# Kernel optimization log

Measured on AMD Instinct MI355X. Metric: run time of the kernel, lower is better.

The kernel has to match this reference:

```python
import jax, jax.numpy as jnp
import numpy as np
import math

LMAX = 2
NUM_Z = 4
N_NODES = 20000
N_GRAPHS = 5000
N_EDGES = 320000
# irreps as (mul, l, parity)
IR_SH   = [(1, 0, 1), (1, 1, -1), (1, 2, 1)]
IR_ATTR = [(NUM_Z**2, 0, 1), (NUM_Z**2, 1, -1), (NUM_Z**2, 2, 1)]
IR_MID  = [(64, 0, 1), (24, 1, 1), (24, 1, -1), (16, 2, 1), (16, 2, -1)]
IR_OUT  = [(1, 0, -1), (6, 0, 1)]


def _cg(j1, j2, j3, m1, m2, m3):
    if m1 + m2 != m3:
        return 0.0
    f = math.factorial
    pre = math.sqrt((2 * j3 + 1) * f(j3 + j1 - j2) * f(j3 - j1 + j2) * f(j1 + j2 - j3) / f(j1 + j2 + j3 + 1))
    pre *= math.sqrt(f(j3 + m3) * f(j3 - m3) * f(j1 - m1) * f(j1 + m1) * f(j2 - m2) * f(j2 + m2))
    s = 0.0
    for k in range(max(0, j2 - j3 - m1, j1 - j3 + m2), min(j1 + j2 - j3, j1 - m1, j2 + m2) + 1):
        s += (-1) ** k / (f(k) * f(j1 + j2 - j3 - k) * f(j1 - m1 - k) * f(j2 + m2 - k) * f(j3 - j2 + m1 + k) * f(j3 - j1 - m2 + k))
    return pre * s


def _u(l):
    # complex -> real spherical harmonics change of basis, m = -l..l
    U = np.zeros((2 * l + 1, 2 * l + 1), dtype=complex)
    for m in range(-l, l + 1):
        if m > 0:
            U[m + l, -m + l] = 1 / math.sqrt(2)
            U[m + l, m + l] = (-1) ** m / math.sqrt(2)
        elif m == 0:
            U[l, l] = 1.0
        else:
            U[m + l, m + l] = 1j / math.sqrt(2)
            U[m + l, -m + l] = -1j * (-1) ** (-m) / math.sqrt(2)
    return U


def _w3j(l1, l2, l3):
    C = np.zeros((2 * l1 + 1, 2 * l2 + 1, 2 * l3 + 1))
    for m1 in range(-l1, l1 + 1):
        for m2 in range(-l2, l2 + 1):
            m3 = m1 + m2
            if -l3 <= m3 <= l3:
                C[m1 + l1, m2 + l2, m3 + l3] = _cg(l1, l2, l3, m1, m2, m3)
    T = np.einsum('am,bn,co,mno->abc', _u(l1), _u(l2), _u(l3).conj(), C.astype(complex))
    T = T.real if np.abs(T.real).max() >= np.abs(T.imag).max() else T.imag
    return (T / np.linalg.norm(T)).astype(np.float32)  # Frobenius norm 1, e3nn convention


W3J = {(a, b, c): _w3j(a, b, c) for a in range(3) for b in range(3) for c in range(3) if abs(a - b) <= c <= a + b}


def _slices(ir):
    s = [0]
    for m, l, _ in ir:
        s.append(s[-1] + m * (2 * l + 1))
    return s


def _paths(ir1, ir2, iro):
    paths = []
    fan = [0] * len(iro)
    off = 0
    for a, (m1, l1, p1) in enumerate(ir1):
        for b, (m2, l2, p2) in enumerate(ir2):
            for c, (m3, l3, p3) in enumerate(iro):
                if p1 * p2 == p3 and abs(l1 - l2) <= l3 <= l1 + l2:
                    paths.append((a, b, c, off))
                    fan[c] += m1 * m2
                    off += m1 * m2 * m3
    return paths, fan, off


def _fctp(x1, x2, w, ir1, ir2, iro):
    # FullyConnectedTensorProduct: 'uvw' weighted Clebsch-Gordan contraction per path
    s1, s2 = _slices(ir1), _slices(ir2)
    paths, fan, _ = _paths(ir1, ir2, iro)
    E = x1.shape[0]
    out = [jnp.zeros((E, m * (2 * l + 1)), x1.dtype) for m, l, _ in iro]
    for a, b, c, off in paths:
        m1, l1, _ = ir1[a]
        m2, l2, _ = ir2[b]
        m3, l3, _ = iro[c]
        W = w[off:off + m1 * m2 * m3].reshape(m1, m2, m3)
        C = jnp.asarray(W3J[(l1, l2, l3)], x1.dtype)
        xa = x1[:, s1[a]:s1[a + 1]].reshape(E, m1, 2 * l1 + 1)
        xb = x2[:, s2[b]:s2[b + 1]].reshape(E, m2, 2 * l2 + 1)
        alpha = math.sqrt(2 * l3 + 1) / math.sqrt(fan[c])
        y = jnp.einsum('eui,evj,ijk,uvw->ewk', xa, xb, C, W)
        out[c] = out[c] + (alpha * y).reshape(E, -1)
    return jnp.concatenate(out, axis=1)


def _sh(v):
    # component-normalized harmonic polynomials for l=0,1,2 (normalize=False)
    x, y, z = v[:, 0], v[:, 1], v[:, 2]
    r2 = x * x + y * y + z * z
    s3, s15, s5 = math.sqrt(3.0), math.sqrt(15.0), math.sqrt(5.0)
    sh1 = s3 * jnp.stack([y, z, x], axis=1)
    sh2 = jnp.stack([s15 * x * y, s15 * y * z, 0.5 * s5 * (3 * z * z - r2), s15 * x * z, 0.5 * s15 * (x * x - y * y)], axis=1)
    return jnp.concatenate([jnp.ones_like(x)[:, None], sh1, sh2], axis=1)  # [E, 9]


def _forward(pos, w_tp1, w_tp2, z, batch, edge_src, edge_dst):
    E = edge_src.shape[0]
    ev = pos[edge_src] - pos[edge_dst]
    sh = _sh(ev)
    zz = NUM_Z * z[edge_src] + z[edge_dst]
    zzf = jax.nn.one_hot(zz, NUM_Z ** 2, dtype=sh.dtype) * NUM_Z  # [E, 16]
    # 'uvu' TensorProduct of (16x0e) with sh: outer product per l block
    blocks = [(0, 1), (1, 4), (4, 9)]
    edge_attr = jnp.concatenate([(zzf[:, :, None] * sh[:, None, a:b]).reshape(E, -1) for a, b in blocks], axis=1)
    inv_nn = 1.0 / math.sqrt(3.0)  # num_neighbors = 3
    node = jax.ops.segment_sum(sh, edge_dst, num_segments=N_NODES) * inv_nn
    ef = _fctp(node[edge_src], edge_attr, w_tp1, IR_SH, IR_ATTR, IR_MID)
    node = jax.ops.segment_sum(ef, edge_dst, num_segments=N_NODES) * inv_nn
    ef = _fctp(node[edge_src], edge_attr, w_tp2, IR_MID, IR_ATTR, IR_OUT)
    node = jax.ops.segment_sum(ef, edge_dst, num_segments=N_NODES) * inv_nn
    return jax.ops.segment_sum(node, batch, num_segments=N_GRAPHS) * 0.5  # num_nodes = 4


def setup_inputs() -> dict:
    key = jax.random.key(0)
    k = jax.random.split(key, 7)
    _, _, n1 = _paths(IR_SH, IR_ATTR, IR_MID)
    _, _, n2 = _paths(IR_MID, IR_ATTR, IR_OUT)
    return {
        'pos': jax.random.normal(k[0], (N_NODES, 3), jnp.float32),
        'z': jax.random.randint(k[1], (N_NODES,), 0, NUM_Z, jnp.int32),
        'batch': jnp.sort(jax.random.randint(k[2], (N_NODES,), 0, N_GRAPHS, jnp.int32)),
        'edge_src': jax.random.randint(k[3], (N_EDGES,), 0, N_NODES, jnp.int32),
        'edge_dst': jax.random.randint(k[4], (N_EDGES,), 0, N_NODES, jnp.int32),
        'w_tp1': jax.random.normal(k[5], (n1,), jnp.float32),
        'w_tp2': jax.random.normal(k[6], (n2,), jnp.float32),
    }


def reference(pos, z, batch, edge_src, edge_dst, w_tp1, w_tp2):
    return _forward(pos, w_tp1, w_tp2, z, batch, edge_src, edge_dst)
```

## Files before the change

### kernel.cpp

```cpp
#include <hip/hip_runtime.h>


#define N_EDGES   320000
#define NN_NODES  20000
#define NN_GRAPHS 5000

__device__ __forceinline__ void sh_from_vec(float x, float y, float z,
                                            float* B1, float* B2) {
    const float s3   = 1.7320508075688772f;
    const float s15  = 3.8729833462074170f;
    const float s5h  = 1.1180339887498949f;
    const float s15h = 1.9364916731037085f;
    B1[0] = s3 * y; B1[1] = s3 * z; B1[2] = s3 * x;
    float r2 = x * x + y * y + z * z;
    B2[0] = s15 * x * y;
    B2[1] = s15 * y * z;
    B2[2] = s5h * (3.f * z * z - r2);
    B2[3] = s15 * x * z;
    B2[4] = s15h * (x * x - y * y);
}

__global__ __launch_bounds__(256) void k_zero(const float* __restrict__ pos,
                                              int* __restrict__ counts,
                                              float* __restrict__ out,
                                              float4* __restrict__ pos4) {
    int tid = blockIdx.x * blockDim.x + threadIdx.x;
    int stride = gridDim.x * blockDim.x;
    for (int i = tid; i < NN_NODES; i += stride) counts[i] = 0;
    for (int i = tid; i < NN_GRAPHS * 7; i += stride) out[i] = 0.f;
    for (int i = tid; i < NN_NODES; i += stride) {
        float4 p;
        p.x = pos[3 * i]; p.y = pos[3 * i + 1]; p.z = pos[3 * i + 2]; p.w = 0.f;
        pos4[i] = p;
    }
}

__global__ __launch_bounds__(256) void k_hist(const int* __restrict__ edst,
                                              int* __restrict__ counts) {
    int e = blockIdx.x * blockDim.x + threadIdx.x;
    if (e < N_EDGES) atomicAdd(&counts[edst[e]], 1);
}

__global__ __launch_bounds__(1024) void k_scan(const int* __restrict__ counts,
                                               int* __restrict__ start,
                                               int* __restrict__ cursor) {
    __shared__ int sdata[1024];
    __shared__ int carry;
    int tid = threadIdx.x;
    if (tid == 0) carry = 0;
    __syncthreads();
    for (int base = 0; base < NN_NODES; base += 1024) {
        int i = base + tid;
        int v = (i < NN_NODES) ? counts[i] : 0;
        sdata[tid] = v;
        __syncthreads();
        for (int off = 1; off < 1024; off <<= 1) {
            int t = (tid >= off) ? sdata[tid - off] : 0;
            __syncthreads();
            sdata[tid] += t;
            __syncthreads();
        }
        int incl = sdata[tid];
        int c = carry;
        if (i < NN_NODES) {
            int excl = c + incl - v;
            start[i] = excl;
            cursor[i] = excl;
        }
        __syncthreads();
        if (tid == 0) carry = c + sdata[1023];
        __syncthreads();
    }
    if (tid == 0) start[NN_NODES] = carry;
}

__global__ __launch_bounds__(256) void k_fill(const int* __restrict__ esrc,
                                              const int* __restrict__ edst,
                                              const int* __restrict__ zarr,
                                              int* __restrict__ cursor,
                                              int* __restrict__ csr) {
    int e = blockIdx.x * blockDim.x + threadIdx.x;
    if (e >= N_EDGES) return;
    int d = edst[e];
    int s = esrc[e];
    int q = 4 * zarr[s] + zarr[d];
    int p = atomicAdd(&cursor[d], 1);
    csr[p] = s | (q << 16) | ((d & 15) << 20);
}

__global__ __launch_bounds__(256) void k_wprep(const float* __restrict__ w2,
                                               float* __restrict__ w2p) {
    const float cT0f =  0.02830690f;
    const float cT1f = -0.02635231f;
    const float cT2f = -0.01634300f;
    const float cT3f =  0.01265893f;
    const float cT4f =  0.02041241f;
    int idx = blockIdx.x * 256 + threadIdx.x;
    if (idx >= 16 * 64 * 64) return;
    int jj = idx & 63;
    int u  = (idx >> 6) & 63;
    int q  = idx >> 12;
    float v = 0.f;
    if (jj < 6) {
        v = cT0f * w2[(u * 16 + q) * 6 + jj];
    } else if (jj < 9) {
        if (u < 24) v = cT1f * w2[6144 + u * 16 + q];
    } else if (jj < 27) {
        int w = (jj - 9) % 6;
        if (u < 24) v = cT2f * w2[6528 + (u * 16 + q) * 6 + w];
    } else if (jj < 57) {
        int w = (jj - 27) % 6;
        if (u < 16) v = cT3f * w2[8832 + (u * 16 + q) * 6 + w];
    } else if (jj < 62) {
        if (u < 16) v = cT4f * w2[10368 + u * 16 + q];
    }
    w2p[idx] = v;
}

__global__ __launch_bounds__(256) void k_nodesh(const float4* __restrict__ pos4,
                                                const int* __restrict__ start,
                                                const int* __restrict__ csr,
                                                float* __restrict__ node_sh) {
    __shared__ float ns[16][12];
    int t = threadIdx.x;
    if (t < 192) ns[t / 12][t % 12] = 0.f;
    __syncthreads();
    int nbase = blockIdx.x * 16;
    int e0 = start[nbase], e1 = start[nbase + 16];
    for (int idx = e0 + t; idx < e1; idx += 256) {
        int pk = csr[idx];
        int s = pk & 0xFFFF;
        int r = (pk >> 20) & 15;
        float4 pd = pos4[nbase + r];
        float4 ps = pos4[s];
        float x = ps.x - pd.x;
        float y = ps.y - pd.y;
        float z = ps.z - pd.z;
        float B1[3], B2[5];
        sh_from_vec(x, y, z, B1, B2);
        float* nr = &ns[r][0];
        atomicAdd(nr + 0, 1.f);
        atomicAdd(nr + 1, B1[0]); atomicAdd(nr + 2, B1[1]); atomicAdd(nr + 3, B1[2]);
        atomicAdd(nr + 4, B2[0]); atomicAdd(nr + 5, B2[1]); atomicAdd(nr + 6, B2[2]);
        atomicAdd(nr + 7, B2[3]); atomicAdd(nr + 8, B2[4]);
    }
    __syncthreads();
    if (t < 144) {
        int r = t / 9, c = t % 9;
        const float inv_nn = 0.57735026918962576f;
        node_sh[(size_t)(nbase + r) * 12 + c] = ns[r][c] * inv_nn;
    }
}

template<int RB>
__device__ __forceinline__ void phase2_pass(const float* __restrict__ Gl,
                                            float (* __restrict__ smid)[368],
                                            const float* __restrict__ w1,
                                            int zpack, int j) {
    const int zp = zpack >> (2 * RB);
    float acc[8] = {0.f, 0.f, 0.f, 0.f, 0.f, 0.f, 0.f, 0.f};
    if (j < 64) {
        int w = j;
        for (int q = 0; q < 16; q++) {
            float wa = w1[q * 64 + w];
            float wb = w1[2048 + q * 64 + w];
            float wc = w1[5248 + q * 64 + w];
            int zdq = q & 3;
            const float* Gq = Gl + (q >> 2) * 51;
#pragma unroll
            for (int r2 = 0; r2 < 8; r2++) {
                if (((zp >> (2 * r2)) & 3) == zdq) {
                    const float* gq = Gq + (RB + r2) * 204;
                    acc[r2] += gq[0] * wa + gq[12] * wb + gq[42] * wc;
                }
            }
        }
#pragma unroll
        for (int r2 = 0; r2 < 8; r2++)
            smid[RB + r2][j] = 0.33333333333333333f * acc[r2];
    } else if (j < 136) {
        int tt = j - 64, w = tt / 3, k = tt - 3 * w;
        for (int q = 0; q < 16; q++) {
            float wa = w1[3072 + q * 24 + w];
            float wb = w1[6272 + q * 24 + w];
            int zdq = q & 3;
            const float* Gq = Gl + (q >> 2) * 51;
#pragma unroll
            for (int r2 = 0; r2 < 8; r2++) {
                if (((zp >> (2 * r2)) & 3) == zdq) {
                    const float* gq = Gq + (RB + r2) * 204;
                    acc[r2] += gq[13 + k] * wa + gq[43 + k] * wb;
                }
            }
        }
#pragma unroll
        for (int r2 = 0; r2 < 8; r2++)
            smid[RB + r2][j] = 0.70710678118654752f * acc[r2];
    } else if (j < 208) {
        int tt = j - 136, w = tt / 3, k = tt - 3 * w;
        for (int q = 0; q < 16; q++) {
            float wa = w1[1024 + q * 24 + w];
            float wb = w1[1664 + q * 24 + w];
            float wc = w1[3712 + q * 24 + w];
            float wd = w1[4608 + q * 24 + w];
            int zdq = q & 3;
            const float* Gq = Gl + (q >> 2) * 51;
#pragma unroll
            for (int r2 = 0; r2 < 8; r2++) {
                if (((zp >> (2 * r2)) & 3) == zdq) {
                    const float* gq = Gq + (RB + r2) * 204;
                    acc[r2] += gq[1 + k] * wa + gq[9 + k] * wb +
                               gq[21 + k] * wc + gq[34 + k] * wd;
                }
            }
        }
#pragma unroll
        for (int r2 = 0; r2 < 8; r2++)
            smid[RB + r2][j] = 0.5f * acc[r2];
    } else if (j < 288) {
        int tt = j - 208, w = tt / 5, k = tt - 5 * w;
        for (int q = 0; q < 16; q++) {
            float wa = w1[1408 + q * 16 + w];
            float wb = w1[3456 + q * 16 + w];
            float wc = w1[4352 + q * 16 + w];
            float wd = w1[6656 + q * 16 + w];
            int zdq = q & 3;
            const float* Gq = Gl + (q >> 2) * 51;
#pragma unroll
            for (int r2 = 0; r2 < 8; r2++) {
                if (((zp >> (2 * r2)) & 3) == zdq) {
                    const float* gq = Gq + (RB + r2) * 204;
                    acc[r2] += gq[4 + k] * wa + gq[16 + k] * wb +
                               gq[29 + k] * wc + gq[46 + k] * wd;
                }
            }
        }
#pragma unroll
        for (int r2 = 0; r2 < 8; r2++)
            smid[RB + r2][j] = 0.64549722436790280f * acc[r2];
    } else if (j < 368) {
        int tt = j - 288, w = tt / 5, k = tt - 5 * w;
        for (int q = 0; q < 16; q++) {
            float wa = w1[4096 + q * 16 + w];
            float wb = w1[4992 + q * 16 + w];
            int zdq = q & 3;
            const float* Gq = Gl + (q >> 2) * 51;
#pragma unroll
            for (int r2 = 0; r2 < 8; r2++) {
                if (((zp >> (2 * r2)) & 3) == zdq) {
                    const float* gq = Gq + (RB + r2) * 204;
                    acc[r2] += gq[24 + k] * wa + gq[37 + k] * wb;
                }
            }
        }
#pragma unroll
        for (int r2 = 0; r2 < 8; r2++)
            smid[RB + r2][j] = 0.91287092917527690f * acc[r2];
    }
}

__global__ __launch_bounds__(512, 4) void k_mid(const float4* __restrict__ pos4,
                                                const float* __restrict__ node_sh,
                                                const int* __restrict__ start,
                                                const int* __restrict__ csr,
                                                const float* __restrict__ w1,
                                                const int* __restrict__ zarr,
                                                const float* __restrict__ w2p,
                                                float* __restrict__ tab) {
    __shared__ float Gl[16 * 204];
    __shared__ float smid[16][368];
    __shared__ int szl[16];
    int t = threadIdx.x;
    int nbase = blockIdx.x * 16;
    for (int i = t; i < 16 * 204; i += 512) Gl[i] = 0.f;
    if (t < 16) szl[t] = zarr[nbase + t];
    __syncthreads();

    int e0 = start[nbase], e1 = start[nbase + 16];

    const float r3  = 0.57735026918962576f;
    const float r5  = 0.44721359549995794f;
    const float r6  = 0.40824829046386302f;
    const float r10 = 0.31622776601683794f;
    const float s30 = 0.18257418583505536f;
    const float rt3 = 1.7320508075688772f;
    const float c222 = 0.58554004376911990f;
    const float q6 = 0.40824829046386302f;
    const float h6 = 0.20412414523193151f;
    const float h2 = 0.35355339059327376f;
    const float r2c = 0.70710678118654752f;

    for (int idx = e0 + t; idx < e1; idx += 512) {
        int pk = csr[idx];
        int s = pk & 0xFFFF;
        int zs = (pk >> 18) & 3;
        int r = (pk >> 20) & 15;
        float4 pd = pos4[nbase + r];
        float4 ps = pos4[s];
        float x = ps.x - pd.x;
        float y = ps.y - pd.y;
        float z = ps.z - pd.z;
        float B1[3], B2[5];
        sh_from_vec(x, y, z, B1, B2);
        const float4 nv0 = *(const float4*)(node_sh + s * 12);
        const float4 nv1 = *(const float4*)(node_sh + s * 12 + 4);
        float a0 = nv0.x;
        float A1[3] = {nv0.y, nv0.z, nv0.w};
        float A2[5] = {nv1.x, nv1.y, nv1.z, nv1.w, node_sh[s * 12 + 8]};
        float* gr = Gl + r * 204 + zs * 51;

        atomicAdd(gr + 0, a0);
        atomicAdd(gr + 1, a0 * B1[0] * r3);
        atomicAdd(gr + 2, a0 * B1[1] * r3);
        atomicAdd(gr + 3, a0 * B1[2] * r3);
        atomicAdd(gr + 4, a0 * B2[0] * r5);
        atomicAdd(gr + 5, a0 * B2[1] * r5);
        atomicAdd(gr + 6, a0 * B2[2] * r5);
        atomicAdd(gr + 7, a0 * B2[3] * r5);
        atomicAdd(gr + 8, a0 * B2[4] * r5);
        atomicAdd(gr + 9,  A1[0] * r3);
        atomicAdd(gr + 10, A1[1] * r3);
        atomicAdd(gr + 11, A1[2] * r3);
        atomicAdd(gr + 12, -r3 * (A1[0] * B1[0] + A1[1] * B1[1] + A1[2] * B1[2]));
        atomicAdd(gr + 13, -r6 * (A1[1] * B1[2] - A1[2] * B1[1]));
        atomicAdd(gr + 14, -r6 * (A1[2] * B1[0] - A1[0] * B1[2]));
        atomicAdd(gr + 15, -r6 * (A1[0] * B1[1] - A1[1] * B1[0]));
        atomicAdd(gr + 16, r10 * (A1[0] * B1[2] + A1[2] * B1[0]));
        atomicAdd(gr + 17, r10 * (A1[0] * B1[1] + A1[1] * B1[0]));
        atomicAdd(gr + 18, s30 * (2.f * A1[1] * B1[1] - A1[0] * B1[0] - A1[2] * B1[2]));
        atomicAdd(gr + 19, r10 * (A1[1] * B1[2] + A1[2] * B1[1]));
        atomicAdd(gr + 20, r10 * (A1[2] * B1[2] - A1[0] * B1[0]));
        {
            float Byy = -B2[2] * q6 - B2[4] * r2c;
            float Bzz = 2.f * B2[2] * q6;
            float Bxx = -B2[2] * q6 + B2[4] * r2c;
            float Bxy = B2[0] * r2c;
            float Byz = B2[1] * r2c;
            float Bxz = B2[3] * r2c;
            atomicAdd(gr + 21, -r5 * (Byy * A1[0] + Byz * A1[1] + Bxy * A1[2]));
            atomicAdd(gr + 22, -r5 * (Byz * A1[0] + Bzz * A1[1] + Bxz * A1[2]));
            atomicAdd(gr + 23, -r5 * (Bxy * A1[0] + Bxz * A1[1] + Bxx * A1[2]));
        }
        atomicAdd(gr + 24, -s30 * (B2[1] * A1[0] - B2[3] * A1[2] + 2.f * B2[4] * A1[1]));
        atomicAdd(gr + 25, -s30 * (-B2[0] * A1[0] - rt3 * B2[2] * A1[2] + B2[3] * A1[1] - B2[4] * A1[2]));
        atomicAdd(gr + 26, -s30 * (rt3 * B2[1] * A1[2] - rt3 * B2[3] * A1[0]));
        atomicAdd(gr + 27, -s30 * (B2[0] * A1[2] - B2[1] * A1[1] + rt3 * B2[2] * A1[0] - B2[4] * A1[0]));
        atomicAdd(gr + 28, -s30 * (-2.f * B2[0] * A1[1] + B2[1] * A1[2] + B2[3] * A1[0]));
        atomicAdd(gr + 29, A2[0] * r5);
        atomicAdd(gr + 30, A2[1] * r5);
        atomicAdd(gr + 31, A2[2] * r5);
        atomicAdd(gr + 32, A2[3] * r5);
        atomicAdd(gr + 33, A2[4] * r5);
        {
            float Ayy = -A2[2] * q6 - A2[4] * r2c;
            float Azz = 2.f * A2[2] * q6;
            float Axx = -A2[2] * q6 + A2[4] * r2c;
            float Axy = A2[0] * r2c;
            float Ayz = A2[1] * r2c;
            float Axz = A2[3] * r2c;
            atomicAdd(gr + 34, -r5 * (Ayy * B1[0] + Ayz * B1[1] + Axy * B1[2]));
            atomicAdd(gr + 35, -r5 * (Ayz * B1[0] + Azz * B1[1] + Axz * B1[2]));
            atomicAdd(gr + 36, -r5 * (Axy * B1[0] + Axz * B1[1] + Axx * B1[2]));
        }
        atomicAdd(gr + 37, s30 * (A2[1] * B1[0] - A2[3] * B1[2] + 2.f * A2[4] * B1[1]));
        atomicAdd(gr + 38, s30 * (-A2[0] * B1[0] - rt3 * A2[2] * B1[2] + A2[3] * B1[1] - A2[4] * B1[2]));
        atomicAdd(gr + 39, s30 * (rt3 * A2[1] * B1[2] - rt3 * A2[3] * B1[0]));
        atomicAdd(gr + 40, s30 * (A2[0] * B1[2] - A2[1] * B1[1] + rt3 * A2[2] * B1[0] - A2[4] * B1[0]));
        atomicAdd(gr + 41, s30 * (-2.f * A2[0] * B1[1] + A2[1] * B1[2] + A2[3] * B1[0]));
        atomicAdd(gr + 42, r5 * (A2[0] * B2[0] + A2[1] * B2[1] + A2[2] * B2[2] +
                                 A2[3] * B2[3] + A2[4] * B2[4]));
        atomicAdd(gr + 43, s30 * (-A2[0] * B2[1] + A2[1] * B2[0] +
                                  rt3 * (A2[2] * B2[3] - A2[3] * B2[2]) +
                                  A2[3] * B2[4] - A2[4] * B2[3]));
        atomicAdd(gr + 44, s30 * (-2.f * A2[0] * B2[4] + 2.f * A2[4] * B2[0] -
                                  A2[1] * B2[3] + A2[3] * B2[1]));
        atomicAdd(gr + 45, s30 * (A2[0] * B2[3] - A2[3] * B2[0] +
                                  rt3 * (A2[1] * B2[2] - A2[2] * B2[1]) +
                                  A2[1] * B2[4] - A2[4] * B2[1]));
        atomicAdd(gr + 46, -c222 * (-q6 * (A2[0] * B2[2] + A2[2] * B2[0]) +
                                    h2 * (A2[1] * B2[3] + A2[3] * B2[1])));
        atomicAdd(gr + 47, -c222 * (h6 * (A2[1] * B2[2] + A2[2] * B2[1]) -
                                    h2 * (A2[1] * B2[4] + A2[4] * B2[1]) +
                                    h2 * (A2[0] * B2[3] + A2[3] * B2[0])));
        atomicAdd(gr + 48, -c222 * (q6 * (A2[2] * B2[2] - A2[0] * B2[0] - A2[4] * B2[4]) +
                                    h6 * (A2[1] * B2[1] + A2[3] * B2[3])));
        atomicAdd(gr + 49, -c222 * (h6 * (A2[3] * B2[2] + A2[2] * B2[3]) +
                                    h2 * (A2[3] * B2[4] + A2[4] * B2[3]) +
                                    h2 * (A2[0] * B2[1] + A2[1] * B2[0])));
        atomicAdd(gr + 50, -c222 * (-q6 * (A2[4] * B2[2] + A2[2] * B2[4]) +
                                    h2 * (A2[3] * B2[3] - A2[1] * B2[1])));
    }
    __syncthreads();

    int zpack = 0;
#pragma unroll
    for (int r2 = 0; r2 < 16; r2++)
        zpack |= __builtin_amdgcn_readfirstlane(szl[r2]) << (2 * r2);

    phase2_pass<0>(Gl, smid, w1, zpack, t);
    phase2_pass<8>(Gl, smid, w1, zpack, t);
    __syncthreads();

    {
        int wave = t >> 6;
        int lane = t & 63;
        int mbase, mstride, ulim;
        if (lane < 6)       { mbase = 0;                mstride = 1; ulim = 64; }
        else if (lane < 9)  { mbase = 64 + (lane - 6);  mstride = 3; ulim = 24; }
        else if (lane < 27) { mbase = 136 + (lane - 9) / 6;  mstride = 3; ulim = 24; }
        else if (lane < 57) { mbase = 208 + (lane - 27) / 6; mstride = 5; ulim = 16; }
        else if (lane < 62) { mbase = 288 + (lane - 57);     mstride = 5; ulim = 16; }
        else                { mbase = 0;                mstride = 0; ulim = 1; }
        int ulim1 = ulim - 1;
#pragma unroll
        for (int rr = 0; rr < 2; rr++) {
            int r = wave * 2 + rr;
            const float* mr = &smid[r][0];
            int zs = (zpack >> (2 * r)) & 3;
            for (int zd = 0; zd < 4; zd++) {
                int q = 4 * zs + zd;
                const float* wp = w2p + (size_t)q * 4096 + lane;
                float s0 = 0.f, s1 = 0.f;
#pragma unroll 8
                for (int u = 0; u < 64; u += 2) {
                    int um0 = (u < ulim) ? u : ulim1;
                    int um1 = (u + 1 < ulim) ? u + 1 : ulim1;
                    s0 += mr[mbase + mstride * um0] * wp[u * 64];
                    s1 += mr[mbase + mstride * um1] * wp[(u + 1) * 64];
                }
                tab[((size_t)(nbase + r) * 4 + zd) * 64 + lane] = s0 + s1;
            }
        }
    }
}

__global__ __launch_bounds__(512, 8) void k_out(const float4* __restrict__ pos4,
                                                const int* __restrict__ zarr,
                                                const int* __restrict__ batch,
                                                const int* __restrict__ start,
                                                const int* __restrict__ csr,
                                                const float* __restrict__ tab,
                                                float* __restrict__ out) {
    int wave = threadIdx.x >> 6;
    int lane = threadIdx.x & 63;
    int n = blockIdx.x * 8 + wave;
    float4 pd = pos4[n];
    int zd = zarr[n];
    int s0 = start[n], s1 = start[n + 1];

    int fsel, oidx;
    if (lane < 6)       { fsel = 0;                  oidx = lane + 1; }
    else if (lane < 9)  { fsel = 1 + (lane - 6);     oidx = 0; }
    else if (lane < 27) { fsel = 1 + (lane - 9) / 6; oidx = (lane - 9) % 6 + 1; }
    else if (lane < 57) { fsel = 4 + (lane - 27) / 6; oidx = (lane - 27) % 6 + 1; }
    else if (lane < 62) { fsel = 4 + (lane - 57);    oidx = 0; }
    else                { fsel = -1;                 oidx = 7; }
    float f0 = (fsel == 0) ? 1.f : 0.f;
    float f1 = (fsel == 1) ? 1.f : 0.f;
    float f2 = (fsel == 2) ? 1.f : 0.f;
    float f3 = (fsel == 3) ? 1.f : 0.f;
    float f4 = (fsel == 4) ? 1.f : 0.f;
    float f5 = (fsel == 5) ? 1.f : 0.f;
    float f6 = (fsel == 6) ? 1.f : 0.f;
    float f7 = (fsel == 7) ? 1.f : 0.f;
    float f8 = (fsel == 8) ? 1.f : 0.f;

    float acc = 0.f;
    for (int idx = s0; idx < s1; ++idx) {
        int pk = csr[idx];
        pk = __builtin_amdgcn_readfirstlane(pk);
        int s = pk & 0xFFFF;
        float T = tab[((size_t)s * 4 + zd) * 64 + lane];
        float4 ps = pos4[s];
        float x = ps.x - pd.x;
        float y = ps.y - pd.y;
        float z = ps.z - pd.z;
        float B1[3], B2[5];
        sh_from_vec(x, y, z, B1, B2);
        float factor = f0 + f1 * B1[0] + f2 * B1[1] + f3 * B1[2]
                     + f4 * B2[0] + f5 * B2[1] + f6 * B2[2]
                     + f7 * B2[3] + f8 * B2[4];
        acc += T * factor;
    }

    float ov[7];
#pragma unroll
    for (int w = 0; w < 7; w++) ov[w] = (oidx == w) ? acc : 0.f;
#pragma unroll
    for (int off = 32; off > 0; off >>= 1)
#pragma unroll
        for (int w = 0; w < 7; w++) ov[w] += __shfl_down(ov[w], off, 64);
    if (lane == 0) {
        float* og = out + batch[n] * 7;
#pragma unroll
        for (int w = 0; w < 7; w++) atomicAdd(og + w, ov[w]);
    }
}

extern "C" void kernel_launch(void* const* d_in, const int* in_sizes, int n_in,
                              void* d_out, int out_size, void* d_ws, size_t ws_size,
                              hipStream_t stream) {
    const float* pos  = (const float*)d_in[0];
    const int*   z    = (const int*)d_in[1];
    const int*   bat  = (const int*)d_in[2];
    const int*   esrc = (const int*)d_in[3];
    const int*   edst = (const int*)d_in[4];
    const float* w1   = (const float*)d_in[5];
    const float* w2   = (const float*)d_in[6];
    float* out = (float*)d_out;

    int*   wsI = (int*)d_ws;
    float* wsF = (float*)d_ws;
    int* counts  = wsI + 0;
    int* start   = wsI + 32768;
    int* cursor  = wsI + 65536;
    int* csr     = wsI + 98304;
    float4* pos4   = (float4*)(wsF + 425984);
    float* node_sh = wsF + 524288;
    float* w2p     = wsF + 786432;
    float* tab     = wsF + 1048576;

    k_zero<<<64, 256, 0, stream>>>(pos, counts, out, pos4);
    k_hist<<<(N_EDGES + 255) / 256, 256, 0, stream>>>(edst, counts);
    k_scan<<<1, 1024, 0, stream>>>(counts, start, cursor);
    k_fill<<<(N_EDGES + 255) / 256, 256, 0, stream>>>(esrc, edst, z, cursor, csr);
    k_wprep<<<256, 256, 0, stream>>>(w2, w2p);
    k_nodesh<<<NN_NODES / 16, 256, 0, stream>>>(pos4, start, csr, node_sh);
    k_mid<<<NN_NODES / 16, 512, 0, stream>>>(pos4, node_sh, start, csr, w1, z, w2p, tab);
    k_out<<<NN_NODES / 8, 512, 0, stream>>>(pos4, z, bat, start, csr, tab, out);
}
```

Baseline: 378.8 us.

## Group nodes by source species to reuse w2p loads across node pairs

The final projection in k_mid now buckets the block's 16 nodes by their source species using shared-memory counters and lists. Each wave processes pairs of same-species nodes and computes all four destination-species outputs together. Every w2p weight load is reused across two nodes and four accumulators instead of being reloaded per node and per zd, cutting global and L2 weight traffic. The cost is more registers, possible imbalance when bucket sizes are odd, and uneven work across waves.

```diff
diff --git a/kernel.cpp b/kernel.cpp
--- a/kernel.cpp
+++ b/kernel.cpp
@@ -270,10 +270,13 @@
     __shared__ float Gl[16 * 204];
     __shared__ float smid[16][368];
     __shared__ int szl[16];
+    __shared__ int zcnt[4];
+    __shared__ int zlist[4][16];
     int t = threadIdx.x;
     int nbase = blockIdx.x * 16;
     for (int i = t; i < 16 * 204; i += 512) Gl[i] = 0.f;
     if (t < 16) szl[t] = zarr[nbase + t];
+    else if (t < 20) zcnt[t - 16] = 0;
     __syncthreads();
 
     int e0 = start[nbase], e1 = start[nbase + 16];
@@ -397,6 +400,12 @@
     for (int r2 = 0; r2 < 16; r2++)
         zpack |= __builtin_amdgcn_readfirstlane(szl[r2]) << (2 * r2);
 
+    if (t < 16) {
+        int zsv = (zpack >> (2 * t)) & 3;
+        int p = atomicAdd(&zcnt[zsv], 1);
+        zlist[zsv][p] = t;
+    }
+
     phase2_pass<0>(Gl, smid, w1, zpack, t);
     phase2_pass<8>(Gl, smid, w1, zpack, t);
     __syncthreads();
@@ -412,23 +421,49 @@
         else if (lane < 62) { mbase = 288 + (lane - 57);     mstride = 5; ulim = 16; }
         else                { mbase = 0;                mstride = 0; ulim = 1; }
         int ulim1 = ulim - 1;
-#pragma unroll
-        for (int rr = 0; rr < 2; rr++) {
-            int r = wave * 2 + rr;
-            const float* mr = &smid[r][0];
-            int zs = (zpack >> (2 * r)) & 3;
-            for (int zd = 0; zd < 4; zd++) {
-                int q = 4 * zs + zd;
-                const float* wp = w2p + (size_t)q * 4096 + lane;
-                float s0 = 0.f, s1 = 0.f;
-#pragma unroll 8
-                for (int u = 0; u < 64; u += 2) {
-                    int um0 = (u < ulim) ? u : ulim1;
-                    int um1 = (u + 1 < ulim) ? u + 1 : ulim1;
-                    s0 += mr[mbase + mstride * um0] * wp[u * 64];
-                    s1 += mr[mbase + mstride * um1] * wp[(u + 1) * 64];
-                }
-                tab[((size_t)(nbase + r) * 4 + zd) * 64 + lane] = s0 + s1;
+
+        int c0 = zcnt[0], c1 = zcnt[1], c2 = zcnt[2], c3 = zcnt[3];
+        int np0 = (c0 + 1) >> 1, np1 = (c1 + 1) >> 1;
+        int np2 = (c2 + 1) >> 1, np3 = (c3 + 1) >> 1;
+        int o1 = np0, o2 = o1 + np1, o3 = o2 + np2;
+        int total = o3 + np3;
+
+        for (int item = wave; item < total; item += 8) {
+            int zsv, pi, cnt;
+            if (item < o1)      { zsv = 0; pi = item;      cnt = c0; }
+            else if (item < o2) { zsv = 1; pi = item - o1; cnt = c1; }
+            else if (item < o3) { zsv = 2; pi = item - o2; cnt = c2; }
+            else                { zsv = 3; pi = item - o3; cnt = c3; }
+            int r0 = zlist[zsv][2 * pi];
+            int i1 = 2 * pi + 1;
+            int has2 = (i1 < cnt);
+            int r1 = has2 ? zlist[zsv][i1] : r0;
+            const float* mr0 = &smid[r0][0];
+            const float* mr1 = &smid[r1][0];
+            const float* wp = w2p + (size_t)(4 * zsv) * 4096 + lane;
+            float a00 = 0.f, a01 = 0.f, a02 = 0.f, a03 = 0.f;
+            float a10 = 0.f, a11 = 0.f, a12 = 0.f, a13 = 0.f;
+#pragma unroll 4
+            for (int u = 0; u < 64; u++) {
+                int um = (u < ulim) ? u : ulim1;
+                float w0 = wp[u * 64];
+                float w1v = wp[4096 + u * 64];
+                float w2v = wp[8192 + u * 64];
+                float w3v = wp[12288 + u * 64];
+                float m0 = mr0[mbase + mstride * um];
+                float m1 = mr1[mbase + mstride * um];
+                a00 += m0 * w0;  a01 += m0 * w1v;
+                a02 += m0 * w2v; a03 += m0 * w3v;
+                a10 += m1 * w0;  a11 += m1 * w1v;
+                a12 += m1 * w2v; a13 += m1 * w3v;
+            }
+            size_t b0 = ((size_t)(nbase + r0) * 4) * 64 + lane;
+            tab[b0] = a00; tab[b0 + 64] = a01;
+            tab[b0 + 128] = a02; tab[b0 + 192] = a03;
+            if (has2) {
+                size_t b1 = ((size_t)(nbase + r1) * 4) * 64 + lane;
+                tab[b1] = a10; tab[b1 + 64] = a11;
+                tab[b1 + 128] = a12; tab[b1 + 192] = a13;
             }
         }
     }
```

Result: no change. 378.4 us (-0.1%).
